# Optimization experiments

Hardware: AMD Instinct MI355X
Metric: run time of the kernel (lower is better)

Reference implementation:

```python
import jax, jax.numpy as jnp
import numpy as np

EMBED_DIM = 1024
N_HEADS = 16
HEAD_DIM = EMBED_DIM // N_HEADS


def setup_inputs() -> dict:
    key = jax.random.key(0)
    k1, k2, k3 = jax.random.split(key, 3)
    B, T, D = 2, 2048, EMBED_DIM
    x = jax.random.normal(k1, (B, T, D), dtype=jnp.float32)
    # torch nn.Linear weights: (out_features, in_features); y = x @ W.T
    scale = 1.0 / np.sqrt(D)
    qkv_w = jax.random.uniform(k2, (3 * D, D), dtype=jnp.float32, minval=-scale, maxval=scale)
    out_w = jax.random.uniform(k3, (D, D), dtype=jnp.float32, minval=-scale, maxval=scale)
    return {"x": x, "qkv_w": qkv_w, "out_w": out_w}


def reference(x, qkv_w, out_w):
    B, T, D = x.shape
    H, hd = N_HEADS, HEAD_DIM
    qkv = jnp.einsum('btd,ed->bte', x, qkv_w)  # (B,T,3D)
    qkv = qkv.reshape(B, T, 3, H, hd)
    q = jnp.transpose(qkv[:, :, 0], (0, 2, 1, 3))  # (B,H,T,hd)
    k = jnp.transpose(qkv[:, :, 1], (0, 2, 1, 3))
    v = jnp.transpose(qkv[:, :, 2], (0, 2, 1, 3))
    scores = jnp.einsum('bhtd,bhsd->bhts', q, k) / np.sqrt(hd).astype(np.float32)
    causal = jnp.tril(jnp.ones((T, T), dtype=bool))  # True = keep
    scores = jnp.where(causal[None, None], scores, -jnp.inf)
    probs = jax.nn.softmax(scores, axis=-1)
    out = jnp.einsum('bhts,bhsd->bhtd', probs, v)
    out = jnp.transpose(out, (0, 2, 1, 3)).reshape(B, T, D)
    return jnp.einsum('btd,ed->bte', out, out_w)
```

## Files before the change

kernel.cpp:

```cpp
#include <hip/hip_runtime.h>
#include <hip/hip_bf16.h>
#include <stdint.h>

typedef __bf16 bf16;
typedef __attribute__((ext_vector_type(8))) __bf16 bf16x8;
typedef __attribute__((ext_vector_type(4))) __bf16 bf16x4;
typedef __attribute__((ext_vector_type(4))) float f32x4;

#define AS1 __attribute__((address_space(1)))
#define AS3 __attribute__((address_space(3)))

__device__ __forceinline__ void async16(const void* g, void* l) {
  __builtin_amdgcn_global_load_lds((AS1 uint32_t*)(g), (AS3 uint32_t*)(l), 16, 0, 0);
}

__device__ __forceinline__ f32x4 mfma_bf16(bf16x8 a, bf16x8 b, f32x4 c) {
  return __builtin_amdgcn_mfma_f32_16x16x32_bf16(a, b, c, 0, 0, 0);
}

__device__ __forceinline__ uint32_t pack2_bf16(float a, float b) {
  union { __hip_bfloat162 h2; uint32_t u; } u;
  u.h2 = __float22bfloat162_rn(float2{a, b});
  return u.u;
}

__global__ __launch_bounds__(256) void cast_all_kernel(
    const float* __restrict__ x, const float* __restrict__ w1,
    const float* __restrict__ w2, bf16* __restrict__ xb,
    bf16* __restrict__ w1b, bf16* __restrict__ w2b) {
  const int bid = blockIdx.x;
  const float* src;
  bf16* dst;
  int base;
  if (bid < 4096) { src = x;  dst = xb;  base = bid; }
  else if (bid < 7168) { src = w1; dst = w1b; base = bid - 4096; }
  else { src = w2; dst = w2b; base = bid - 7168; }
  const int i = (base * 256 + threadIdx.x) * 4;
  const float4 v = *(const float4*)(src + i);
  bf16x4 o;
  o[0] = (bf16)v.x; o[1] = (bf16)v.y; o[2] = (bf16)v.z; o[3] = (bf16)v.w;
  *(bf16x4*)(dst + i) = o;
}

__global__ __launch_bounds__(256) void gemm_qkv_kernel(
    const bf16* __restrict__ A, const bf16* __restrict__ W,
    bf16* __restrict__ QK, bf16* __restrict__ VT) {
  constexpr int K = 1024;
  __shared__ __align__(16) bf16 sm[2 * 128 * 32];
  const int tid = threadIdx.x;
  const int w = tid >> 6, lane = tid & 63;
  const int m0 = blockIdx.x * 128, n0 = blockIdx.y * 128;
  const int wm = (w >> 1) * 64, wn = (w & 1) * 64;
  const int lrow = lane & 15, quad = lane >> 4;
  const int lk = quad * 8;
  f32x4 acc[4][4] = {};

  for (int k0 = 0; k0 < K; k0 += 32) {
#pragma unroll
    for (int i = 0; i < 4; ++i) {
      const int c = tid + 256 * i;
      const bf16* src = (c < 512)
          ? (A + (size_t)(m0 + (c >> 2)) * K + k0 + (c & 3) * 8)
          : (W + (size_t)(n0 + ((c - 512) >> 2)) * K + k0 + (c & 3) * 8);
      async16(src, sm + (w * 64 + i * 256) * 8);
    }
    __syncthreads();
    bf16x8 af[4], bfr[4];
#pragma unroll
    for (int mi = 0; mi < 4; ++mi)
      af[mi] = *(const bf16x8*)&sm[(wm + mi * 16 + lrow) * 32 + lk];
#pragma unroll
    for (int ni = 0; ni < 4; ++ni)
      bfr[ni] = *(const bf16x8*)&sm[128 * 32 + (wn + ni * 16 + lrow) * 32 + lk];
#pragma unroll
    for (int mi = 0; mi < 4; ++mi)
#pragma unroll
      for (int ni = 0; ni < 4; ++ni)
        acc[mi][ni] = mfma_bf16(af[mi], bfr[ni], acc[mi][ni]);
    __syncthreads();
  }

  bf16* s2 = sm;
  const bool isV = (n0 >= 2048);
  const int bb = m0 >> 11;
  const int mt = m0 & 2047;
  if (!isV) {
#pragma unroll
    for (int c = 0; c < 2; ++c) {
      if ((w >> 1) == c) {
#pragma unroll
        for (int mi = 0; mi < 4; ++mi)
#pragma unroll
          for (int ni = 0; ni < 4; ++ni) {
            const int nr = wn + ni * 16 + lrow;
#pragma unroll
            for (int r = 0; r < 4; ++r)
              s2[(mi * 16 + quad * 4 + r) * 128 + nr] = (bf16)acc[mi][ni][r];
          }
      }
      __syncthreads();
#pragma unroll
      for (int p = 0; p < 4; ++p) {
        const int row = p * 16 + (tid >> 4);
        const int colc = (tid & 15) * 8;
        const bf16x8 v = *(const bf16x8*)&s2[row * 128 + colc];
        *(bf16x8*)(QK + (size_t)(m0 + c * 64 + row) * 2048 + n0 + colc) = v;
      }
      __syncthreads();
    }
  } else {
#pragma unroll
    for (int c = 0; c < 2; ++c) {
      if ((w & 1) == c) {
#pragma unroll
        for (int mi = 0; mi < 4; ++mi)
#pragma unroll
          for (int ni = 0; ni < 4; ++ni) {
            const int nl = ni * 16 + lrow;
            bf16x4 pk4;
#pragma unroll
            for (int r = 0; r < 4; ++r) pk4[r] = (bf16)acc[mi][ni][r];
            *(bf16x4*)&s2[nl * 128 + wm + mi * 16 + quad * 4] = pk4;
          }
      }
      __syncthreads();
#pragma unroll
      for (int p = 0; p < 4; ++p) {
        const int row = p * 16 + (tid >> 4);
        const int colc = (tid & 15) * 8;
        const bf16x8 v = *(const bf16x8*)&s2[row * 128 + colc];
        const int vtrow = bb * 1024 + (n0 - 2048) + c * 64 + row;
        *(bf16x8*)(VT + (size_t)vtrow * 2048 + mt + colc) = v;
      }
      __syncthreads();
    }
  }
}

__global__ __launch_bounds__(512) void attn_kernel(
    const bf16* __restrict__ QK, const bf16* __restrict__ VT,
    bf16* __restrict__ AO) {
  __shared__ __align__(16) bf16 sK[2][2][64 * 64];
  __shared__ __align__(16) bf16 sV[2][2][64 * 64];
  const int bid = blockIdx.x;
  const int bh = bid & 31;
  const int bp = bid >> 5;
  const int b = bh >> 4, h = bh & 15;
  const int tid = threadIdx.x, w = tid >> 6, lane = tid & 63;
  const int col = lane & 15, quad = lane >> 4;
  const bf16* Qb = QK + (size_t)b * 2048 * 2048 + h * 64;
  const bf16* Kb = Qb + 1024;
  const bf16* Vb = VT + (size_t)bh * 64 * 2048;
  const float NEG_INF = -__builtin_inff();
  constexpr float QSCALE = 0.18033688011112042f;
  const int n0 = 16 - bp;

  union { uint32_t u[4]; bf16x8 v; } ones;
  ones.u[0] = 0x3F803F80u; ones.u[1] = 0x3F803F80u;
  ones.u[2] = 0x3F803F80u; ones.u[3] = 0x3F803F80u;

  const int R0a = (15 - bp) * 128 + w * 16;
  const int R0b = bp * 128 + w * 16;
  const int qrow0 = R0a + col, qrow1 = R0b + col;
  bf16x8 qf0[2], qf1[2];
#pragma unroll
  for (int kk = 0; kk < 2; ++kk) {
    bf16x8 v0 = *(const bf16x8*)(Qb + (size_t)qrow0 * 2048 + kk * 32 + quad * 8);
    bf16x8 v1 = *(const bf16x8*)(Qb + (size_t)qrow1 * 2048 + kk * 32 + quad * 8);
#pragma unroll
    for (int e = 0; e < 8; ++e) {
      v0[e] = (bf16)((float)v0[e] * QSCALE);
      v1[e] = (bf16)((float)v1[e] * QSCALE);
    }
    qf0[kk] = v0; qf1[kk] = v1;
  }

  auto stage = [&](int s0, int cur) {
    bf16* dK = &sK[cur][0][0];
    bf16* dV = &sV[cur][0][0];
#pragma unroll
    for (int i = 0; i < 2; ++i) {
      const int L = tid + 512 * i;
      const int buf = L >> 9, Lr = L & 511;
      const int row = Lr >> 3;
      const int ch = (Lr & 7) ^ (row & 7);
      async16(Kb + (size_t)(s0 + buf * 64 + row) * 2048 + ch * 8, dK + L * 8);
    }
#pragma unroll
    for (int i = 0; i < 2; ++i) {
      const int L = tid + 512 * i;
      const int buf = L >> 9, Lr = L & 511;
      const int d = Lr >> 3;
      const int ch = (Lr & 7) ^ (d & 7);
      async16(Vb + (size_t)d * 2048 + s0 + buf * 64 + ch * 8, dV + L * 8);
    }
  };

  int srow[4];
#pragma unroll
  for (int m = 0; m < 4; ++m)
    srow[m] = 32 * (m & 1) + (col >> 2) * 8 + 4 * (m >> 1) + (col & 3);

  f32x4 accO[4] = {};
  f32x4 accL = {};

  auto body = [&](const bf16* kbuf, const bf16* vbuf, bf16x8 qa, bf16x8 qb,
                  int kv0, int qrowv, bool masked) {
    f32x4 st[4] = {};
    const bf16x8 qfl[2] = {qa, qb};
#pragma unroll
    for (int kk = 0; kk < 2; ++kk) {
      bf16x8 kf[4];
#pragma unroll
      for (int m = 0; m < 4; ++m)
        kf[m] = *(const bf16x8*)&kbuf[srow[m] * 64 + (((kk * 4 + quad) ^ (srow[m] & 7)) * 8)];
      __builtin_amdgcn_s_setprio(1);
#pragma unroll
      for (int m = 0; m < 4; ++m)
        st[m] = mfma_bf16(kf[m], qfl[kk], st[m]);
      __builtin_amdgcn_s_setprio(0);
    }

    if (masked) {
#pragma unroll
      for (int m = 0; m < 4; ++m) {
        const int kvb = kv0 + 32 * (m & 1) + quad * 8 + 4 * (m >> 1);
#pragma unroll
        for (int r = 0; r < 4; ++r)
          st[m][r] = (kvb + r <= qrowv) ? st[m][r] : NEG_INF;
      }
    }

    uint32_t pk[4][2];
#pragma unroll
    for (int m = 0; m < 4; ++m) {
      const float p0 = __builtin_amdgcn_exp2f(st[m][0]);
      const float p1 = __builtin_amdgcn_exp2f(st[m][1]);
      const float p2 = __builtin_amdgcn_exp2f(st[m][2]);
      const float p3 = __builtin_amdgcn_exp2f(st[m][3]);
      pk[m][0] = pack2_bf16(p0, p1);
      pk[m][1] = pack2_bf16(p2, p3);
    }

#pragma unroll
    for (int kk = 0; kk < 2; ++kk) {
      bf16x8 vf[4];
#pragma unroll
      for (int d = 0; d < 4; ++d) {
        const int row = d * 16 + col;
        vf[d] = *(const bf16x8*)&vbuf[row * 64 + (((kk * 4 + quad) ^ (row & 7)) * 8)];
      }
      union { uint32_t u[4]; bf16x8 v; } f;
      f.u[0] = pk[kk][0];
      f.u[1] = pk[kk][1];
      f.u[2] = pk[2 + kk][0];
      f.u[3] = pk[2 + kk][1];
      __builtin_amdgcn_s_setprio(1);
      accL = mfma_bf16(ones.v, f.v, accL);
#pragma unroll
      for (int d = 0; d < 4; ++d)
        accO[d] = mfma_bf16(vf[d], f.v, accO[d]);
      __builtin_amdgcn_s_setprio(0);
    }
  };

  auto runpair = [&](int j, int cur, bf16x8 qa, bf16x8 qb, int qrowv, int R0w) {
    const int kv0 = j * 128;
    if (kv0 <= R0w + 15)
      body(&sK[cur][0][0], &sV[cur][0][0], qa, qb, kv0, qrowv, kv0 + 63 > R0w);
    if (kv0 + 64 <= R0w + 15)
      body(&sK[cur][1][0], &sV[cur][1][0], qa, qb, kv0 + 64, qrowv, kv0 + 127 > R0w);
  };

  auto writeout = [&](int qrowv) {
    bf16* Ob = AO + (size_t)b * 2048 * 1024 + h * 64;
    const float inv = 1.0f / accL[0];
#pragma unroll
    for (int d = 0; d < 4; ++d) {
      bf16x4 o;
#pragma unroll
      for (int r = 0; r < 4; ++r) o[r] = (bf16)(accO[d][r] * inv);
      *(bf16x4*)(Ob + (size_t)qrowv * 1024 + d * 16 + quad * 4) = o;
    }
  };

  stage(0, 0);
  int cur = 0;
  for (int i = 0; i < 17; ++i) {
    if (i + 1 < 17) {
      const int nx = (i + 1 < n0) ? (i + 1) : (i + 1 - n0);
      stage(nx * 128, cur ^ 1);
      asm volatile("s_waitcnt vmcnt(4)" ::: "memory");
    } else {
      asm volatile("s_waitcnt vmcnt(0)" ::: "memory");
    }
    __builtin_amdgcn_s_barrier();
    if (i < n0) runpair(i, cur, qf0[0], qf0[1], qrow0, R0a);
    else        runpair(i - n0, cur, qf1[0], qf1[1], qrow1, R0b);
    if (i == n0 - 1) {
      writeout(qrow0);
#pragma unroll
      for (int d = 0; d < 4; ++d) accO[d] = f32x4{0.f, 0.f, 0.f, 0.f};
      accL = f32x4{0.f, 0.f, 0.f, 0.f};
    }
    __builtin_amdgcn_s_barrier();
    cur ^= 1;
  }
  writeout(qrow1);
}

__global__ __launch_bounds__(256) void gemm_out_kernel(
    const bf16* __restrict__ A, const bf16* __restrict__ W,
    float* __restrict__ C) {
  constexpr int K = 1024;
  __shared__ __align__(16) bf16 sm[2 * 128 * 32];
  const int tid = threadIdx.x;
  const int w = tid >> 6, lane = tid & 63;
  const int m0 = blockIdx.x * 128, n0 = blockIdx.y * 128;
  const int wm = (w >> 1) * 64, wn = (w & 1) * 64;
  const int lrow = lane & 15, lk = (lane >> 4) * 8;
  f32x4 acc[4][4] = {};

  for (int k0 = 0; k0 < K; k0 += 32) {
#pragma unroll
    for (int i = 0; i < 4; ++i) {
      const int c = tid + 256 * i;
      const bf16* src = (c < 512)
          ? (A + (size_t)(m0 + (c >> 2)) * K + k0 + (c & 3) * 8)
          : (W + (size_t)(n0 + ((c - 512) >> 2)) * K + k0 + (c & 3) * 8);
      async16(src, sm + (w * 64 + i * 256) * 8);
    }
    __syncthreads();
    bf16x8 af[4], bfr[4];
#pragma unroll
    for (int mi = 0; mi < 4; ++mi)
      af[mi] = *(const bf16x8*)&sm[(wm + mi * 16 + lrow) * 32 + lk];
#pragma unroll
    for (int ni = 0; ni < 4; ++ni)
      bfr[ni] = *(const bf16x8*)&sm[128 * 32 + (wn + ni * 16 + lrow) * 32 + lk];
#pragma unroll
    for (int mi = 0; mi < 4; ++mi)
#pragma unroll
      for (int ni = 0; ni < 4; ++ni)
        acc[mi][ni] = mfma_bf16(af[mi], bfr[ni], acc[mi][ni]);
    __syncthreads();
  }

#pragma unroll
  for (int mi = 0; mi < 4; ++mi)
#pragma unroll
    for (int ni = 0; ni < 4; ++ni) {
      const int n = n0 + wn + ni * 16 + lrow;
#pragma unroll
      for (int r = 0; r < 4; ++r) {
        const int m = m0 + wm + mi * 16 + (lane >> 4) * 4 + r;
        C[(size_t)m * 1024 + n] = acc[mi][ni][r];
      }
    }
}

extern "C" void kernel_launch(void* const* d_in, const int* in_sizes, int n_in,
                              void* d_out, int out_size, void* d_ws, size_t ws_size,
                              hipStream_t stream) {
  const float* x     = (const float*)d_in[0];
  const float* qkv_w = (const float*)d_in[1];
  const float* out_w = (const float*)d_in[2];
  float* out = (float*)d_out;

  char* ws = (char*)d_ws;
  bf16* xb    = (bf16*)(ws);
  bf16* aob   = (bf16*)(ws);
  bf16* wqkvb = (bf16*)(ws + 8u * 1024 * 1024);
  bf16* wob   = (bf16*)(ws + 14u * 1024 * 1024);
  bf16* qkb   = (bf16*)(ws + 16u * 1024 * 1024);
  bf16* vtb   = (bf16*)(ws + 32u * 1024 * 1024);

  cast_all_kernel<<<8192, 256, 0, stream>>>(x, qkv_w, out_w, xb, wqkvb, wob);
  gemm_qkv_kernel<<<dim3(32, 24), 256, 0, stream>>>(xb, wqkvb, qkb, vtb);
  attn_kernel<<<dim3(256), 512, 0, stream>>>(qkb, vtb, aob);
  gemm_out_kernel<<<dim3(32, 8), 256, 0, stream>>>(aob, wob, out);
}
```

Measured before the change: 172.5 us.

## Switch attention to 32x32x16 MFMA with 4 waves of 32 query rows

Rewrites the attention kernel to use 32x32x16 bf16 MFMA tiles, so each of 4 waves (256 threads instead of 512) handles 32 query rows against 64-key tiles. P is rearranged between the S and PV MFMAs with v_permlane32_swap instead of matching layouts through LDS ordering. The larger tiles cut LDS fragment loads per FLOP, at the cost of half as many waves per block, fewer waves to hide latency, and scalar bf16 output stores.

```diff
diff --git a/kernel.cpp b/kernel.cpp
--- a/kernel.cpp
+++ b/kernel.cpp
@@ -6,6 +6,7 @@
 typedef __attribute__((ext_vector_type(8))) __bf16 bf16x8;
 typedef __attribute__((ext_vector_type(4))) __bf16 bf16x4;
 typedef __attribute__((ext_vector_type(4))) float f32x4;
+typedef __attribute__((ext_vector_type(16))) float f32x16;
 
 #define AS1 __attribute__((address_space(1)))
 #define AS3 __attribute__((address_space(3)))
@@ -16,6 +17,10 @@
 
 __device__ __forceinline__ f32x4 mfma_bf16(bf16x8 a, bf16x8 b, f32x4 c) {
   return __builtin_amdgcn_mfma_f32_16x16x32_bf16(a, b, c, 0, 0, 0);
+}
+
+__device__ __forceinline__ f32x16 mfma32(bf16x8 a, bf16x8 b, f32x16 c) {
+  return __builtin_amdgcn_mfma_f32_32x32x16_bf16(a, b, c, 0, 0, 0);
 }
 
 __device__ __forceinline__ uint32_t pack2_bf16(float a, float b) {
@@ -137,7 +142,7 @@
   }
 }
 
-__global__ __launch_bounds__(512) void attn_kernel(
+__global__ __launch_bounds__(256) void attn_kernel(
     const bf16* __restrict__ QK, const bf16* __restrict__ VT,
     bf16* __restrict__ AO) {
   __shared__ __align__(16) bf16 sK[2][2][64 * 64];
@@ -145,50 +150,49 @@
   const int bid = blockIdx.x;
   const int bh = bid & 31;
   const int bp = bid >> 5;
-  const int b = bh >> 4, h = bh & 15;
+  const int b = bh >> 4, hd = bh & 15;
   const int tid = threadIdx.x, w = tid >> 6, lane = tid & 63;
-  const int col = lane & 15, quad = lane >> 4;
-  const bf16* Qb = QK + (size_t)b * 2048 * 2048 + h * 64;
+  const int ln31 = lane & 31, hf = lane >> 5;
+  const bf16* Qb = QK + (size_t)b * 2048 * 2048 + hd * 64;
   const bf16* Kb = Qb + 1024;
   const bf16* Vb = VT + (size_t)bh * 64 * 2048;
   const float NEG_INF = -__builtin_inff();
   constexpr float QSCALE = 0.18033688011112042f;
   const int n0 = 16 - bp;
+  const int RH = (15 - bp) * 128 + w * 32;
+  const int RL = bp * 128 + w * 32;
 
   union { uint32_t u[4]; bf16x8 v; } ones;
   ones.u[0] = 0x3F803F80u; ones.u[1] = 0x3F803F80u;
   ones.u[2] = 0x3F803F80u; ones.u[3] = 0x3F803F80u;
 
-  const int R0a = (15 - bp) * 128 + w * 16;
-  const int R0b = bp * 128 + w * 16;
-  const int qrow0 = R0a + col, qrow1 = R0b + col;
-  bf16x8 qf0[2], qf1[2];
-#pragma unroll
-  for (int kk = 0; kk < 2; ++kk) {
-    bf16x8 v0 = *(const bf16x8*)(Qb + (size_t)qrow0 * 2048 + kk * 32 + quad * 8);
-    bf16x8 v1 = *(const bf16x8*)(Qb + (size_t)qrow1 * 2048 + kk * 32 + quad * 8);
+  bf16x8 qfH[4], qfL[4];
+#pragma unroll
+  for (int ks = 0; ks < 4; ++ks) {
+    bf16x8 v0 = *(const bf16x8*)(Qb + (size_t)(RH + ln31) * 2048 + ks * 16 + hf * 8);
+    bf16x8 v1 = *(const bf16x8*)(Qb + (size_t)(RL + ln31) * 2048 + ks * 16 + hf * 8);
 #pragma unroll
     for (int e = 0; e < 8; ++e) {
       v0[e] = (bf16)((float)v0[e] * QSCALE);
       v1[e] = (bf16)((float)v1[e] * QSCALE);
     }
-    qf0[kk] = v0; qf1[kk] = v1;
-  }
-
-  auto stage = [&](int s0, int cur) {
-    bf16* dK = &sK[cur][0][0];
-    bf16* dV = &sV[cur][0][0];
-#pragma unroll
-    for (int i = 0; i < 2; ++i) {
-      const int L = tid + 512 * i;
+    qfH[ks] = v0; qfL[ks] = v1;
+  }
+
+  auto stage = [&](int s0, int c) {
+    bf16* dK = &sK[c][0][0];
+    bf16* dV = &sV[c][0][0];
+#pragma unroll
+    for (int i2 = 0; i2 < 4; ++i2) {
+      const int L = tid + 256 * i2;
       const int buf = L >> 9, Lr = L & 511;
       const int row = Lr >> 3;
       const int ch = (Lr & 7) ^ (row & 7);
       async16(Kb + (size_t)(s0 + buf * 64 + row) * 2048 + ch * 8, dK + L * 8);
     }
 #pragma unroll
-    for (int i = 0; i < 2; ++i) {
-      const int L = tid + 512 * i;
+    for (int i2 = 0; i2 < 4; ++i2) {
+      const int L = tid + 256 * i2;
       const int buf = L >> 9, Lr = L & 511;
       const int d = Lr >> 3;
       const int ch = (Lr & 7) ^ (d & 7);
@@ -196,91 +200,77 @@
     }
   };
 
-  int srow[4];
-#pragma unroll
-  for (int m = 0; m < 4; ++m)
-    srow[m] = 32 * (m & 1) + (col >> 2) * 8 + 4 * (m >> 1) + (col & 3);
-
-  f32x4 accO[4] = {};
-  f32x4 accL = {};
-
-  auto body = [&](const bf16* kbuf, const bf16* vbuf, bf16x8 qa, bf16x8 qb,
-                  int kv0, int qrowv, bool masked) {
-    f32x4 st[4] = {};
-    const bf16x8 qfl[2] = {qa, qb};
-#pragma unroll
-    for (int kk = 0; kk < 2; ++kk) {
-      bf16x8 kf[4];
-#pragma unroll
-      for (int m = 0; m < 4; ++m)
-        kf[m] = *(const bf16x8*)&kbuf[srow[m] * 64 + (((kk * 4 + quad) ^ (srow[m] & 7)) * 8)];
-      __builtin_amdgcn_s_setprio(1);
-#pragma unroll
-      for (int m = 0; m < 4; ++m)
-        st[m] = mfma_bf16(kf[m], qfl[kk], st[m]);
-      __builtin_amdgcn_s_setprio(0);
-    }
-
-    if (masked) {
-#pragma unroll
-      for (int m = 0; m < 4; ++m) {
-        const int kvb = kv0 + 32 * (m & 1) + quad * 8 + 4 * (m >> 1);
-#pragma unroll
-        for (int r = 0; r < 4; ++r)
-          st[m][r] = (kvb + r <= qrowv) ? st[m][r] : NEG_INF;
-      }
-    }
-
-    uint32_t pk[4][2];
-#pragma unroll
-    for (int m = 0; m < 4; ++m) {
-      const float p0 = __builtin_amdgcn_exp2f(st[m][0]);
-      const float p1 = __builtin_amdgcn_exp2f(st[m][1]);
-      const float p2 = __builtin_amdgcn_exp2f(st[m][2]);
-      const float p3 = __builtin_amdgcn_exp2f(st[m][3]);
-      pk[m][0] = pack2_bf16(p0, p1);
-      pk[m][1] = pack2_bf16(p2, p3);
-    }
-
-#pragma unroll
-    for (int kk = 0; kk < 2; ++kk) {
-      bf16x8 vf[4];
-#pragma unroll
-      for (int d = 0; d < 4; ++d) {
-        const int row = d * 16 + col;
-        vf[d] = *(const bf16x8*)&vbuf[row * 64 + (((kk * 4 + quad) ^ (row & 7)) * 8)];
-      }
-      union { uint32_t u[4]; bf16x8 v; } f;
-      f.u[0] = pk[kk][0];
-      f.u[1] = pk[kk][1];
-      f.u[2] = pk[2 + kk][0];
-      f.u[3] = pk[2 + kk][1];
-      __builtin_amdgcn_s_setprio(1);
-      accL = mfma_bf16(ones.v, f.v, accL);
-#pragma unroll
-      for (int d = 0; d < 4; ++d)
-        accO[d] = mfma_bf16(vf[d], f.v, accO[d]);
-      __builtin_amdgcn_s_setprio(0);
+  f32x16 accO0 = {}, accO1 = {};
+  f32x16 accL = {};
+
+  auto body = [&](const bf16* kbuf, const bf16* vbuf, const bf16x8 (&qf)[4],
+                  int kv0, int R, bool masked) {
+    f32x16 st0 = {}, st1 = {};
+#pragma unroll
+    for (int ks = 0; ks < 4; ++ks) {
+      const int ch = (((2 * ks + hf) ^ (ln31 & 7)) * 8);
+      const bf16x8 kf0 = *(const bf16x8*)&kbuf[ln31 * 64 + ch];
+      const bf16x8 kf1 = *(const bf16x8*)&kbuf[(32 + ln31) * 64 + ch];
+      st0 = mfma32(kf0, qf[ks], st0);
+      st1 = mfma32(kf1, qf[ks], st1);
+    }
+    const int q = R + ln31;
+    float p0[16], p1[16];
+#pragma unroll
+    for (int r = 0; r < 16; ++r) {
+      const int crow = (r & 3) + 8 * (r >> 2) + 4 * hf;
+      float s0 = st0[r], s1 = st1[r];
+      if (masked) {
+        s0 = (kv0 + crow <= q) ? s0 : NEG_INF;
+        s1 = (kv0 + 32 + crow <= q) ? s1 : NEG_INF;
+      }
+      p0[r] = __builtin_amdgcn_exp2f(s0);
+      p1[r] = __builtin_amdgcn_exp2f(s1);
+    }
+    bf16x8 pa[4];
+#pragma unroll
+    for (int mt = 0; mt < 2; ++mt) {
+#pragma unroll
+      for (int ksl = 0; ksl < 2; ++ksl) {
+        const int bs = ksl * 8;
+        uint32_t x0, y0, x1, y1;
+        if (mt == 0) {
+          x0 = pack2_bf16(p0[bs + 0], p0[bs + 1]);
+          y0 = pack2_bf16(p0[bs + 4], p0[bs + 5]);
+          x1 = pack2_bf16(p0[bs + 2], p0[bs + 3]);
+          y1 = pack2_bf16(p0[bs + 6], p0[bs + 7]);
+        } else {
+          x0 = pack2_bf16(p1[bs + 0], p1[bs + 1]);
+          y0 = pack2_bf16(p1[bs + 4], p1[bs + 5]);
+          x1 = pack2_bf16(p1[bs + 2], p1[bs + 3]);
+          y1 = pack2_bf16(p1[bs + 6], p1[bs + 7]);
+        }
+        asm volatile("v_permlane32_swap_b32 %0, %1" : "+v"(x0), "+v"(y0));
+        asm volatile("v_permlane32_swap_b32 %0, %1" : "+v"(x1), "+v"(y1));
+        union { uint32_t u[4]; bf16x8 v; } f;
+        f.u[0] = x0; f.u[1] = x1; f.u[2] = y0; f.u[3] = y1;
+        pa[mt * 2 + ksl] = f.v;
+      }
+    }
+#pragma unroll
+    for (int ks = 0; ks < 4; ++ks) {
+      const int ch = (((2 * ks + hf) ^ (ln31 & 7)) * 8);
+      const bf16x8 vf0 = *(const bf16x8*)&vbuf[ln31 * 64 + ch];
+      const bf16x8 vf1 = *(const bf16x8*)&vbuf[(32 + ln31) * 64 + ch];
+      accO0 = mfma32(pa[ks], vf0, accO0);
+      accO1 = mfma32(pa[ks], vf1, accO1);
+      accL  = mfma32(pa[ks], ones.v, accL);
     }
   };
 
-  auto runpair = [&](int j, int cur, bf16x8 qa, bf16x8 qb, int qrowv, int R0w) {
-    const int kv0 = j * 128;
-    if (kv0 <= R0w + 15)
-      body(&sK[cur][0][0], &sV[cur][0][0], qa, qb, kv0, qrowv, kv0 + 63 > R0w);
-    if (kv0 + 64 <= R0w + 15)
-      body(&sK[cur][1][0], &sV[cur][1][0], qa, qb, kv0 + 64, qrowv, kv0 + 127 > R0w);
-  };
-
-  auto writeout = [&](int qrowv) {
-    bf16* Ob = AO + (size_t)b * 2048 * 1024 + h * 64;
-    const float inv = 1.0f / accL[0];
-#pragma unroll
-    for (int d = 0; d < 4; ++d) {
-      bf16x4 o;
-#pragma unroll
-      for (int r = 0; r < 4; ++r) o[r] = (bf16)(accO[d][r] * inv);
-      *(bf16x4*)(Ob + (size_t)qrowv * 1024 + d * 16 + quad * 4) = o;
+  auto writeout = [&](int R) {
+    bf16* Ob = AO + (size_t)b * 2048 * 1024 + hd * 64;
+#pragma unroll
+    for (int r = 0; r < 16; ++r) {
+      const int qr = R + (r & 3) + 8 * (r >> 2) + 4 * hf;
+      const float inv = 1.0f / accL[r];
+      Ob[(size_t)qr * 1024 + ln31]      = (bf16)(accO0[r] * inv);
+      Ob[(size_t)qr * 1024 + 32 + ln31] = (bf16)(accO1[r] * inv);
     }
   };
 
@@ -290,23 +280,32 @@
     if (i + 1 < 17) {
       const int nx = (i + 1 < n0) ? (i + 1) : (i + 1 - n0);
       stage(nx * 128, cur ^ 1);
-      asm volatile("s_waitcnt vmcnt(4)" ::: "memory");
+      asm volatile("s_waitcnt vmcnt(8)" ::: "memory");
     } else {
       asm volatile("s_waitcnt vmcnt(0)" ::: "memory");
     }
     __builtin_amdgcn_s_barrier();
-    if (i < n0) runpair(i, cur, qf0[0], qf0[1], qrow0, R0a);
-    else        runpair(i - n0, cur, qf1[0], qf1[1], qrow1, R0b);
-    if (i == n0 - 1) {
-      writeout(qrow0);
-#pragma unroll
-      for (int d = 0; d < 4; ++d) accO[d] = f32x4{0.f, 0.f, 0.f, 0.f};
-      accL = f32x4{0.f, 0.f, 0.f, 0.f};
+    if (i < n0) {
+      const int kv0 = i * 128;
+      if (kv0 <= RH + 31)
+        body(&sK[cur][0][0], &sV[cur][0][0], qfH, kv0, RH, kv0 + 63 > RH);
+      if (kv0 + 64 <= RH + 31)
+        body(&sK[cur][1][0], &sV[cur][1][0], qfH, kv0 + 64, RH, kv0 + 127 > RH);
+      if (i == n0 - 1) {
+        writeout(RH);
+        accO0 = f32x16{}; accO1 = f32x16{}; accL = f32x16{};
+      }
+    } else {
+      const int kv0 = (i - n0) * 128;
+      if (kv0 <= RL + 31)
+        body(&sK[cur][0][0], &sV[cur][0][0], qfL, kv0, RL, kv0 + 63 > RL);
+      if (kv0 + 64 <= RL + 31)
+        body(&sK[cur][1][0], &sV[cur][1][0], qfL, kv0 + 64, RL, kv0 + 127 > RL);
     }
     __builtin_amdgcn_s_barrier();
     cur ^= 1;
   }
-  writeout(qrow1);
+  writeout(RL);
 }
 
 __global__ __launch_bounds__(256) void gemm_out_kernel(
@@ -377,6 +376,6 @@
 
   cast_all_kernel<<<8192, 256, 0, stream>>>(x, qkv_w, out_w, xb, wqkvb, wob);
   gemm_qkv_kernel<<<dim3(32, 24), 256, 0, stream>>>(xb, wqkvb, qkb, vtb);
-  attn_kernel<<<dim3(256), 512, 0, stream>>>(qkb, vtb, aob);
+  attn_kernel<<<dim3(256), 256, 0, stream>>>(qkb, vtb, aob);
   gemm_out_kernel<<<dim3(32, 8), 256, 0, stream>>>(aob, wob, out);
 }
```

New measurement: 196.0 us. 1.14x slower.
